# Optimization experiments

Measured on AMD Instinct MI355X. Metric: run time of the kernel, lower is better.

## Reference

```python
import jax, jax.numpy as jnp
import numpy as np

K = 5          # kernel size (hard-coded in feature_propogate)
DIL = 2        # dilation
PAD = (K + (DIL - 1) * (K - 1)) // 2  # = 4, same-padding for unfold


def _unfold_w_center(x):
    """torch F.unfold(kernel=5, dilation=2, padding=4) reshaped to [B,C,25,H,W].
    Neighbor index n is kernel row-major (ki*5+kj), matching torch unfold."""
    B, C, H, W = x.shape
    p = jnp.pad(x, ((0, 0), (0, 0), (PAD, PAD), (PAD, PAD)))
    nb = jnp.stack(
        [p[:, :, DIL * i: DIL * i + H, DIL * j: DIL * j + W]
         for i in range(K) for j in range(K)],
        axis=2,
    )  # [B, C, 25, H, W]
    return nb


def setup_inputs() -> dict:
    key = jax.random.key(0)
    k1, k2 = jax.random.split(key)
    feat = jax.random.normal(k1, (4, 128, 128, 128), dtype=jnp.float32) * 0.1
    w_cls = jax.random.normal(k2, (1, 128), dtype=jnp.float32) * 0.1
    b_cls = jnp.zeros((1,), dtype=jnp.float32)
    return {"feat": feat, "w_cls": w_cls, "b_cls": b_cls}


def reference(feat, w_cls, b_cls):
    # feature_propogate: unfold-based local self-attention over 5x5 dilated nbhd
    nb = _unfold_w_center(feat)                          # [B,C,25,H,W]
    corr = jnp.einsum('bchw,bcnhw->bhwn', feat, nb)      # correlation
    attn = jax.nn.softmax(jnp.maximum(corr, 0.0), -1)    # clamp(min=0) + softmax
    prop = jnp.einsum('bcnhw,bhwn->bchw', nb, attn)      # weighted gather-sum
    # 1x1 classifier (Conv2d(C, num_classes, 1))
    logits = jnp.einsum('bchw,oc->bohw', prop, w_cls) + b_cls[None, :, None, None]
    return logits
```

## Files before the change

### kernel.cpp

```cpp
#include <hip/hip_runtime.h>

#define C 128
#define H 128
#define W 128
#define HW (H*W)

__global__ __launch_bounds__(640, 4) void fused_kernel(
    const float* __restrict__ feat, const float* __restrict__ wc,
    const float* __restrict__ bc, float* __restrict__ out)
{
    __shared__ float corr_s[2][25][W];
    __shared__ float g_s[2][5][W];
    __shared__ float wc_s[C];

    const int blk0 = blockIdx.x;
    const int blk  = (blk0 & 7) * 64 + (blk0 >> 3);
    const int b    = blk >> 7;
    const int r    = blk & 127;
    const int tid  = threadIdx.x;
    const int wv   = tid >> 6;
    const int ti   = wv >> 1;
    const int h    = wv & 1;
    const int lane = tid & 63;
    const int s    = lane >> 5;
    const int pg   = lane & 31;
    const int w0   = pg * 4;

    if (tid < C) wc_s[tid] = wc[tid];
    __syncthreads();

    const int  rt  = r - 4 + 2 * ti;
    const bool rok = (unsigned)rt < (unsigned)H;

    float acc[5][4];
    float ga[4];
#pragma unroll
    for (int j = 0; j < 5; ++j)
#pragma unroll
        for (int p = 0; p < 4; ++p) acc[j][p] = 0.f;
#pragma unroll
    for (int p = 0; p < 4; ++p) ga[p] = 0.f;

    if (rok) {
        int sb[3];
#pragma unroll
        for (int t = 0; t < 3; ++t) {
            const int cs = w0 - 4 + 4 * t;
            sb[t] = cs < 0 ? 0 : (cs > W - 4 ? W - 4 : cs);
        }
        const float* fbase = feat + ((size_t)(b * C + h * 64 + s * 32)) * HW;
        const float* tp = fbase + rt * W;
        const float* cp = fbase + r * W + w0;
        const int wci = h * 64 + s * 32;

#pragma unroll 2
        for (int c = 0; c < 32; ++c) {
            const float4 A  = *(const float4*)(tp + sb[0]);
            const float4 Bv = *(const float4*)(tp + sb[1]);
            const float4 Cv = *(const float4*)(tp + sb[2]);
            const float4 D  = *(const float4*)cp;
            const float wcv = wc_s[wci + c];

            const float win[12] = {A.x, A.y, A.z, A.w,
                                   Bv.x, Bv.y, Bv.z, Bv.w,
                                   Cv.x, Cv.y, Cv.z, Cv.w};
            const float ctr[4] = {D.x, D.y, D.z, D.w};

#pragma unroll
            for (int p = 0; p < 4; ++p)
                ga[p] = fmaf(wcv, win[4 + p], ga[p]);
#pragma unroll
            for (int j = 0; j < 5; ++j)
#pragma unroll
                for (int p = 0; p < 4; ++p)
                    acc[j][p] = fmaf(ctr[p], win[p + 2 * j], acc[j][p]);

            tp += HW; cp += HW;
        }
    }

#pragma unroll
    for (int j = 0; j < 5; ++j)
#pragma unroll
        for (int p = 0; p < 4; ++p)
            acc[j][p] += __shfl_xor(acc[j][p], 32);
#pragma unroll
    for (int p = 0; p < 4; ++p) ga[p] += __shfl_xor(ga[p], 32);

    if (s == 0) {
#pragma unroll
        for (int j = 0; j < 5; ++j)
#pragma unroll
            for (int p = 0; p < 4; ++p) {
                const int  col = w0 + p - 4 + 2 * j;
                const bool ok  = rok && ((unsigned)col < (unsigned)W);
                corr_s[h][ti * 5 + j][w0 + p] = ok ? acc[j][p] : 0.f;
            }
#pragma unroll
        for (int p = 0; p < 4; ++p) g_s[h][ti][w0 + p] = ga[p];
    }
    __syncthreads();

    if (tid < W) {
        const int w = tid;
        float v[25], m = 0.f;
#pragma unroll
        for (int n = 0; n < 25; ++n) {
            v[n] = fmaxf(corr_s[0][n][w] + corr_s[1][n][w], 0.f);
            m = fmaxf(m, v[n]);
        }
        float sum = 0.f, num = 0.f;
#pragma unroll
        for (int i = 0; i < 5; ++i) {
            const bool riv = (unsigned)(r - 4 + 2 * i) < (unsigned)H;
#pragma unroll
            for (int j = 0; j < 5; ++j) {
                const float e = __expf(v[i * 5 + j] - m);
                sum += e;
                const int  wt = w - 4 + 2 * j;
                const bool ok = riv && ((unsigned)wt < (unsigned)W);
                const int  wi = ok ? wt : 0;
                const float gv = g_s[0][i][wi] + g_s[1][i][wi];
                num = fmaf(e, ok ? gv : 0.f, num);
            }
        }
        out[((size_t)(b * H + r)) * W + w] = num / sum + bc[0];
    }
}

extern "C" void kernel_launch(void* const* d_in, const int* in_sizes, int n_in,
                              void* d_out, int out_size, void* d_ws, size_t ws_size,
                              hipStream_t stream) {
    const float* feat = (const float*)d_in[0];
    const float* wcls = (const float*)d_in[1];
    const float* bcls = (const float*)d_in[2];
    float* outp = (float*)d_out;

    fused_kernel<<<dim3(4 * H), dim3(640), 0, stream>>>(feat, wcls, bcls, outp);
}
```

Before: 94.34 us.

## Replace neighbor window loads with lane shuffles and batch channel loads

Each lane now loads only its own float4 of the target row and gets the left and right neighbor float4s from adjacent lanes through shuffles, instead of issuing three overlapping global loads. Center-row threads reuse the target load as the center vector, and four channels are loaded per iteration to raise memory-level parallelism. Launch bounds are raised to five blocks per CU. The shuffles add ALU and cross-lane cost. Boundary lanes receive values from the other 32-lane half instead of clamped reads, which relies on the later column masking being correct.

```diff
diff --git a/kernel.cpp b/kernel.cpp
--- a/kernel.cpp
+++ b/kernel.cpp
@@ -5,7 +5,7 @@
 #define W 128
 #define HW (H*W)
 
-__global__ __launch_bounds__(640, 4) void fused_kernel(
+__global__ __launch_bounds__(640, 5) void fused_kernel(
     const float* __restrict__ feat, const float* __restrict__ wc,
     const float* __restrict__ bc, float* __restrict__ out)
 {
@@ -42,40 +42,54 @@
     for (int p = 0; p < 4; ++p) ga[p] = 0.f;
 
     if (rok) {
-        int sb[3];
+        const float* fbase = feat + ((size_t)(b * C + h * 64 + s * 32)) * HW;
+        const float* tp = fbase + rt * W + w0;
+        const float* cp = fbase + r  * W + w0;
+        const int wci = h * 64 + s * 32;
+        const bool isCtr = (ti == 2);
+
+#pragma unroll 1
+        for (int cc = 0; cc < 32; cc += 4) {
+            float4 T[4], D[4];
 #pragma unroll
-        for (int t = 0; t < 3; ++t) {
-            const int cs = w0 - 4 + 4 * t;
-            sb[t] = cs < 0 ? 0 : (cs > W - 4 ? W - 4 : cs);
-        }
-        const float* fbase = feat + ((size_t)(b * C + h * 64 + s * 32)) * HW;
-        const float* tp = fbase + rt * W;
-        const float* cp = fbase + r * W + w0;
-        const int wci = h * 64 + s * 32;
-
-#pragma unroll 2
-        for (int c = 0; c < 32; ++c) {
-            const float4 A  = *(const float4*)(tp + sb[0]);
-            const float4 Bv = *(const float4*)(tp + sb[1]);
-            const float4 Cv = *(const float4*)(tp + sb[2]);
-            const float4 D  = *(const float4*)cp;
-            const float wcv = wc_s[wci + c];
-
-            const float win[12] = {A.x, A.y, A.z, A.w,
-                                   Bv.x, Bv.y, Bv.z, Bv.w,
-                                   Cv.x, Cv.y, Cv.z, Cv.w};
-            const float ctr[4] = {D.x, D.y, D.z, D.w};
-
+            for (int u = 0; u < 4; ++u)
+                T[u] = *(const float4*)(tp + (cc + u) * HW);
+            if (isCtr) {
 #pragma unroll
-            for (int p = 0; p < 4; ++p)
-                ga[p] = fmaf(wcv, win[4 + p], ga[p]);
+                for (int u = 0; u < 4; ++u) D[u] = T[u];
+            } else {
 #pragma unroll
-            for (int j = 0; j < 5; ++j)
+                for (int u = 0; u < 4; ++u)
+                    D[u] = *(const float4*)(cp + (cc + u) * HW);
+            }
+#pragma unroll
+            for (int u = 0; u < 4; ++u) {
+                const float wcv = wc_s[wci + cc + u];
+                const float ctr[4] = {D[u].x, D[u].y, D[u].z, D[u].w};
+                float win[12];
+                win[4] = T[u].x; win[5] = T[u].y; win[6] = T[u].z; win[7] = T[u].w;
+                win[0]  = __shfl_up(T[u].x, 1);
+                win[1]  = __shfl_up(T[u].y, 1);
+                win[2]  = __shfl_up(T[u].z, 1);
+                win[3]  = __shfl_up(T[u].w, 1);
+                win[8]  = __shfl_down(T[u].x, 1);
+                win[9]  = __shfl_down(T[u].y, 1);
+                win[10] = __shfl_down(T[u].z, 1);
+                win[11] = __shfl_down(T[u].w, 1);
 #pragma unroll
                 for (int p = 0; p < 4; ++p)
-                    acc[j][p] = fmaf(ctr[p], win[p + 2 * j], acc[j][p]);
-
-            tp += HW; cp += HW;
+                    ga[p] = fmaf(wcv, win[4 + p], ga[p]);
+#pragma unroll
+                for (int p = 0; p < 4; ++p)
+                    acc[2][p] = fmaf(ctr[p], win[4 + p], acc[2][p]);
+#pragma unroll
+                for (int j = 0; j < 5; ++j) {
+                    if (j == 2) continue;
+#pragma unroll
+                    for (int p = 0; p < 4; ++p)
+                        acc[j][p] = fmaf(ctr[p], win[p + 2 * j], acc[j][p]);
+                }
+            }
         }
     }
 
```

New measurement: 96.40 us. 2.2% more time.

## Split fused kernel into channel-split correlation kernel and separate softmax kernel

Applied to the files above, without the earlier changes.

Each correlation block now covers half the channels (1024 blocks instead of 512), with 16 channels per thread. Partial correlations and classifier projections go to workspace memory, and a second kernel reduces them and applies softmax. The classifier projection is computed only by the center-row waves and reuses the loaded window instead of reloading. The aim is more parallelism and occupancy, at the cost of a second launch and a global round trip for the intermediate correlations (about 13 MB).

```diff
diff --git a/kernel.cpp b/kernel.cpp
--- a/kernel.cpp
+++ b/kernel.cpp
@@ -5,41 +5,36 @@
 #define W 128
 #define HW (H*W)
 
-__global__ __launch_bounds__(640, 4) void fused_kernel(
+__global__ __launch_bounds__(640, 8) void corr_kernel(
     const float* __restrict__ feat, const float* __restrict__ wc,
-    const float* __restrict__ bc, float* __restrict__ out)
+    float* __restrict__ corrG, float* __restrict__ gG)
 {
     __shared__ float corr_s[2][25][W];
-    __shared__ float g_s[2][5][W];
-    __shared__ float wc_s[C];
+    __shared__ float g_s[2][W];
 
     const int blk0 = blockIdx.x;
-    const int blk  = (blk0 & 7) * 64 + (blk0 >> 3);
-    const int b    = blk >> 7;
-    const int r    = blk & 127;
+    const int blk  = (blk0 & 7) * 128 + (blk0 >> 3);
+    const int b    = blk >> 8;
+    const int r    = (blk >> 1) & 127;
+    const int h    = blk & 1;
     const int tid  = threadIdx.x;
     const int wv   = tid >> 6;
     const int ti   = wv >> 1;
-    const int h    = wv & 1;
+    const int q    = wv & 1;
     const int lane = tid & 63;
     const int s    = lane >> 5;
     const int pg   = lane & 31;
     const int w0   = pg * 4;
 
-    if (tid < C) wc_s[tid] = wc[tid];
-    __syncthreads();
-
     const int  rt  = r - 4 + 2 * ti;
     const bool rok = (unsigned)rt < (unsigned)H;
 
     float acc[5][4];
-    float ga[4];
+    float ga[4] = {0.f, 0.f, 0.f, 0.f};
 #pragma unroll
     for (int j = 0; j < 5; ++j)
 #pragma unroll
         for (int p = 0; p < 4; ++p) acc[j][p] = 0.f;
-#pragma unroll
-    for (int p = 0; p < 4; ++p) ga[p] = 0.f;
 
     if (rok) {
         int sb[3];
@@ -48,33 +43,34 @@
             const int cs = w0 - 4 + 4 * t;
             sb[t] = cs < 0 ? 0 : (cs > W - 4 ? W - 4 : cs);
         }
-        const float* fbase = feat + ((size_t)(b * C + h * 64 + s * 32)) * HW;
-        const float* tp = fbase + rt * W;
-        const float* cp = fbase + r * W + w0;
-        const int wci = h * 64 + s * 32;
+        const int cbase = h * 64 + q * 32 + s * 16;
+        const float* tp = feat + ((size_t)(b * C + cbase) * H + rt) * W;
+        const float* cp = feat + ((size_t)(b * C + cbase) * H + r ) * W + w0;
+        const bool isCtr = (ti == 2);
 
-#pragma unroll 2
-        for (int c = 0; c < 32; ++c) {
+#pragma unroll 1
+        for (int c = 0; c < 16; ++c) {
             const float4 A  = *(const float4*)(tp + sb[0]);
             const float4 Bv = *(const float4*)(tp + sb[1]);
             const float4 Cv = *(const float4*)(tp + sb[2]);
-            const float4 D  = *(const float4*)cp;
-            const float wcv = wc_s[wci + c];
-
+            float4 D;
+            if (isCtr) D = Bv;
+            else       D = *(const float4*)cp;
+            const float wcv = wc[cbase + c];
             const float win[12] = {A.x, A.y, A.z, A.w,
                                    Bv.x, Bv.y, Bv.z, Bv.w,
                                    Cv.x, Cv.y, Cv.z, Cv.w};
             const float ctr[4] = {D.x, D.y, D.z, D.w};
-
+            if (isCtr) {
 #pragma unroll
-            for (int p = 0; p < 4; ++p)
-                ga[p] = fmaf(wcv, win[4 + p], ga[p]);
+                for (int p = 0; p < 4; ++p)
+                    ga[p] = fmaf(wcv, win[4 + p], ga[p]);
+            }
 #pragma unroll
             for (int j = 0; j < 5; ++j)
 #pragma unroll
                 for (int p = 0; p < 4; ++p)
                     acc[j][p] = fmaf(ctr[p], win[p + 2 * j], acc[j][p]);
-
             tp += HW; cp += HW;
         }
     }
@@ -84,8 +80,10 @@
 #pragma unroll
         for (int p = 0; p < 4; ++p)
             acc[j][p] += __shfl_xor(acc[j][p], 32);
+    if (ti == 2) {
 #pragma unroll
-    for (int p = 0; p < 4; ++p) ga[p] += __shfl_xor(ga[p], 32);
+        for (int p = 0; p < 4; ++p) ga[p] += __shfl_xor(ga[p], 32);
+    }
 
     if (s == 0) {
 #pragma unroll
@@ -94,38 +92,63 @@
             for (int p = 0; p < 4; ++p) {
                 const int  col = w0 + p - 4 + 2 * j;
                 const bool ok  = rok && ((unsigned)col < (unsigned)W);
-                corr_s[h][ti * 5 + j][w0 + p] = ok ? acc[j][p] : 0.f;
+                corr_s[q][ti * 5 + j][w0 + p] = ok ? acc[j][p] : 0.f;
             }
+        if (ti == 2) {
 #pragma unroll
-        for (int p = 0; p < 4; ++p) g_s[h][ti][w0 + p] = ga[p];
+            for (int p = 0; p < 4; ++p) g_s[q][w0 + p] = ga[p];
+        }
     }
     __syncthreads();
 
-    if (tid < W) {
-        const int w = tid;
-        float v[25], m = 0.f;
+    float* cg = corrG + (size_t)blk * (25 * W);
+    const float* s0 = &corr_s[0][0][0];
+    const float* s1 = &corr_s[1][0][0];
+    for (int idx = tid; idx < 25 * W; idx += 640)
+        cg[idx] = s0[idx] + s1[idx];
+    if (tid < W)
+        gG[(size_t)blk * W + tid] = g_s[0][tid] + g_s[1][tid];
+}
+
+__global__ __launch_bounds__(128) void soft_kernel(
+    const float* __restrict__ corrG, const float* __restrict__ gG,
+    const float* __restrict__ bc, float* __restrict__ out)
+{
+    const int blk0 = blockIdx.x;
+    const int xcd  = blk0 & 7;
+    const int idx  = blk0 >> 3;
+    const int b    = xcd >> 1;
+    const int r    = (xcd & 1) * 64 + idx;
+    const int w    = threadIdx.x;
+
+    const size_t base = ((size_t)(b * H + r)) * 2;
+    const float* c0 = corrG + base * (25 * W);
+    const float* c1 = c0 + (25 * W);
+
+    float v[25], m = 0.f;
 #pragma unroll
-        for (int n = 0; n < 25; ++n) {
-            v[n] = fmaxf(corr_s[0][n][w] + corr_s[1][n][w], 0.f);
-            m = fmaxf(m, v[n]);
+    for (int n = 0; n < 25; ++n) {
+        v[n] = fmaxf(c0[n * W + w] + c1[n * W + w], 0.f);
+        m = fmaxf(m, v[n]);
+    }
+    float sum = 0.f, num = 0.f;
+#pragma unroll
+    for (int i = 0; i < 5; ++i) {
+        const int  rt  = r - 4 + 2 * i;
+        const bool riv = (unsigned)rt < (unsigned)H;
+        const size_t gb = ((size_t)(b * H + (riv ? rt : 0))) * 2 * W;
+#pragma unroll
+        for (int j = 0; j < 5; ++j) {
+            const float e = __expf(v[i * 5 + j] - m);
+            sum += e;
+            const int  wt = w - 4 + 2 * j;
+            const bool ok = riv && ((unsigned)wt < (unsigned)W);
+            const int  wi = ok ? wt : 0;
+            const float gv = gG[gb + wi] + gG[gb + W + wi];
+            num = fmaf(e, ok ? gv : 0.f, num);
         }
-        float sum = 0.f, num = 0.f;
-#pragma unroll
-        for (int i = 0; i < 5; ++i) {
-            const bool riv = (unsigned)(r - 4 + 2 * i) < (unsigned)H;
-#pragma unroll
-            for (int j = 0; j < 5; ++j) {
-                const float e = __expf(v[i * 5 + j] - m);
-                sum += e;
-                const int  wt = w - 4 + 2 * j;
-                const bool ok = riv && ((unsigned)wt < (unsigned)W);
-                const int  wi = ok ? wt : 0;
-                const float gv = g_s[0][i][wi] + g_s[1][i][wi];
-                num = fmaf(e, ok ? gv : 0.f, num);
-            }
-        }
-        out[((size_t)(b * H + r)) * W + w] = num / sum + bc[0];
     }
+    out[((size_t)(b * H + r)) * W + w] = num / sum + bc[0];
 }
 
 extern "C" void kernel_launch(void* const* d_in, const int* in_sizes, int n_in,
@@ -134,7 +157,10 @@
     const float* feat = (const float*)d_in[0];
     const float* wcls = (const float*)d_in[1];
     const float* bcls = (const float*)d_in[2];
-    float* outp = (float*)d_out;
+    float* outp  = (float*)d_out;
+    float* corrG = (float*)d_ws;
+    float* gG    = corrG + (size_t)1024 * 25 * W;
 
-    fused_kernel<<<dim3(4 * H), dim3(640), 0, stream>>>(feat, wcls, bcls, outp);
+    corr_kernel<<<dim3(1024), dim3(640), 0, stream>>>(feat, wcls, corrG, gG);
+    soft_kernel<<<dim3(512), dim3(128), 0, stream>>>(corrG, gG, bcls, outp);
 }
```

Result: slower. 101.9 us (+8.1%).
